# Kernel optimization log

Measured on AMD Instinct MI355X. Metric: run time of the kernel, lower is better.

## Reference

```python
import jax, jax.numpy as jnp
import numpy as np

HEADS = 16
DIM_HEAD = 64
SCALE = DIM_HEAD ** -0.5


def setup_inputs() -> dict:
    key = jax.random.key(0)
    k1, k2, k3, k4 = jax.random.split(key, 4)
    b, n, dim = 2, 2048, 1024
    inner = HEADS * DIM_HEAD  # 1024
    x = jax.random.normal(k1, (b, n, dim), dtype=jnp.float32)
    mask = jax.random.randint(k2, (b, n), 0, 2, dtype=jnp.int32)
    Wqkv = jax.random.normal(k3, (dim, inner), dtype=jnp.float32) * (dim ** -0.5)
    Wout = jax.random.normal(k4, (inner, dim), dtype=jnp.float32) * (inner ** -0.5)
    bout = jnp.zeros((dim,), dtype=jnp.float32)
    return {"x": x, "mask": mask, "Wqkv": Wqkv, "Wout": Wout, "bout": bout}


def reference(x, mask, Wqkv, Wout, bout):
    b, n, _ = x.shape
    # shared projection: w acts as q = k = v (CRATE subspace attention)
    w = jnp.einsum('bnd,de->bne', x, Wqkv)
    w = w.reshape(b, n, HEADS, DIM_HEAD).transpose(0, 2, 1, 3)  # b h n d
    dots = jnp.einsum('bhid,bhjd->bhij', w, w) * SCALE           # b h n n
    attn = jax.nn.softmax(dots, axis=-1)
    # post-softmax multiplicative masking (mask=1 zeros the column)
    m = mask[:, None, None, :].astype(attn.dtype)
    attn = attn * (1.0 - m)
    out = jnp.einsum('bhij,bhjd->bhid', attn, w)                 # b h n d
    out = out.transpose(0, 2, 1, 3).reshape(b, n, HEADS * DIM_HEAD)
    return jnp.einsum('bne,ed->bnd', out, Wout) + bout
```

## Files before the change

kernel.cpp:

```cpp
#include <hip/hip_runtime.h>
#include <hip/hip_bf16.h>
#include <stdint.h>

typedef unsigned short u16;
typedef unsigned int u32;
typedef __bf16 bf16x8 __attribute__((ext_vector_type(8)));
typedef float f32x4 __attribute__((ext_vector_type(4)));
typedef float f32x16 __attribute__((ext_vector_type(16)));
typedef u32 u32x4 __attribute__((ext_vector_type(4)));

#define AS1 __attribute__((address_space(1)))
#define AS3 __attribute__((address_space(3)))

__device__ __forceinline__ void async16(const u16* g, u16* l) {
  __builtin_amdgcn_global_load_lds((const AS1 uint32_t*)(const void*)g,
                                   (AS3 uint32_t*)l, 16, 0, 0);
}

__device__ __forceinline__ u16 f2bf(float v) {
  union { __hip_bfloat16 b; u16 u; } c; c.b = __float2bfloat16(v); return c.u;
}

__device__ __forceinline__ u32 pkbf(float a, float b) {
  u32 r;
  asm("v_cvt_pk_bf16_f32 %0, %1, %2" : "=v"(r) : "v"(a), "v"(b));
  return r;
}

__device__ __forceinline__ void swap32(u32 &a, u32 &b) {
  asm("v_permlane32_swap_b32 %0, %1" : "+v"(a), "+v"(b));
}

#if __has_builtin(__builtin_amdgcn_exp2f)
#define fast_exp2(x) __builtin_amdgcn_exp2f(x)
#else
#define fast_exp2(x) exp2f(x)
#endif

#if __has_builtin(__builtin_amdgcn_rcpf)
#define fast_rcp(x) __builtin_amdgcn_rcpf(x)
#else
#define fast_rcp(x) (1.0f / (x))
#endif

__device__ __forceinline__ uint4 pack8(float4 lo, float4 hi) {
  uint4 q;
  q.x = (u32)f2bf(lo.x) | ((u32)f2bf(lo.y) << 16);
  q.y = (u32)f2bf(lo.z) | ((u32)f2bf(lo.w) << 16);
  q.z = (u32)f2bf(hi.x) | ((u32)f2bf(hi.y) << 16);
  q.w = (u32)f2bf(hi.z) | ((u32)f2bf(hi.w) << 16);
  return q;
}

__global__ void prep(const float* __restrict__ x, u16* __restrict__ xb,
                     const float* __restrict__ Wqkv, u16* __restrict__ WqkvT,
                     const float* __restrict__ Wout, u16* __restrict__ WoutT) {
  const int tx = threadIdx.x, ty = threadIdx.y, z = blockIdx.z;
  if (z >= 2) {
    const int cid = (z - 2) * 256 + blockIdx.y * 16 + blockIdx.x;
    const int t = ty * 16 + tx;
    const int i = (cid * 256 + t) * 8;
    float4 lo = *(const float4*)(x + i);
    float4 hi = *(const float4*)(x + i + 4);
    *(uint4*)(xb + i) = pack8(lo, hi);
    return;
  }
  const float* in = z ? Wout : Wqkv;
  u16* out = z ? WoutT : WqkvT;
  __shared__ u16 tile[64][65];
  const int c0 = blockIdx.x * 64, r0 = blockIdx.y * 64;
#pragma unroll
  for (int i = 0; i < 4; i++) {
    const int row = r0 + ty + i * 16;
    float4 v = *(const float4*)&in[(size_t)row * 1024 + c0 + tx * 4];
    tile[tx * 4 + 0][ty + i * 16] = f2bf(v.x);
    tile[tx * 4 + 1][ty + i * 16] = f2bf(v.y);
    tile[tx * 4 + 2][ty + i * 16] = f2bf(v.z);
    tile[tx * 4 + 3][ty + i * 16] = f2bf(v.w);
  }
  __syncthreads();
#pragma unroll
  for (int i = 0; i < 4; i++) {
    const int orow = c0 + ty + i * 16;
    u32 w0 = (u32)tile[ty + i * 16][tx * 4 + 0] | ((u32)tile[ty + i * 16][tx * 4 + 1] << 16);
    u32 w1 = (u32)tile[ty + i * 16][tx * 4 + 2] | ((u32)tile[ty + i * 16][tx * 4 + 3] << 16);
    uint2 pk = {w0, w1};
    *(uint2*)&out[(size_t)orow * 1024 + r0 + tx * 4] = pk;
  }
}

__global__ void scale_transpose_v(const u16* __restrict__ w, const int* __restrict__ mask,
                                  u16* __restrict__ Vt) {
  __shared__ u16 tile[64][65];
  const int tx = threadIdx.x, ty = threadIdx.y;
  const int j0 = blockIdx.x * 64;
  const int bh = blockIdx.z, b = bh >> 4, hc = (bh & 15) * 64;
#pragma unroll
  for (int i = 0; i < 4; i++) {
    const int j = j0 + ty + i * 16;
    uint2 v = *(const uint2*)&w[(size_t)(b * 2048 + j) * 1024 + hc + tx * 4];
    if (mask[b * 2048 + j]) { v.x = 0u; v.y = 0u; }
    tile[tx * 4 + 0][ty + i * 16] = (u16)(v.x & 0xFFFF);
    tile[tx * 4 + 1][ty + i * 16] = (u16)(v.x >> 16);
    tile[tx * 4 + 2][ty + i * 16] = (u16)(v.y & 0xFFFF);
    tile[tx * 4 + 3][ty + i * 16] = (u16)(v.y >> 16);
  }
  __syncthreads();
#pragma unroll
  for (int i = 0; i < 4; i++) {
    const int d = ty + i * 16;
    u32 w0 = (u32)tile[d][tx * 4 + 0] | ((u32)tile[d][tx * 4 + 1] << 16);
    u32 w1 = (u32)tile[d][tx * 4 + 2] | ((u32)tile[d][tx * 4 + 3] << 16);
    uint2 pk = {w0, w1};
    *(uint2*)&Vt[((size_t)bh * 64 + d) * 2048 + j0 + tx * 4] = pk;
  }
}

template<bool OUT_F32>
__launch_bounds__(256)
__global__ void gemm_bt(const u16* __restrict__ A, const u16* __restrict__ BT,
                        void* __restrict__ Cp, const float* __restrict__ bias,
                        int M, int N, int K) {
  __shared__ __align__(16) u16 As[2][64 * 64];
  __shared__ __align__(16) u16 Bs[2][64 * 64];
  const int t = threadIdx.x;
  const int lane = t & 63, wave = t >> 6;
  const int ql = lane & 31, hi = lane >> 5, swz = ql & 7;
  const int wgid = blockIdx.x + gridDim.x * blockIdx.y;
  const int c = wgid & 7, ii = wgid >> 3;
  const int m0 = (c * 8 + (ii & 7)) * 64;
  const int n0 = (ii >> 3) * 64;
  const int wm = (wave & 1) * 32, wn = (wave >> 1) * 32;

  f32x16 acc = {};

  const int sr = t >> 3;
  const int sc8 = ((t & 7) ^ (sr & 7)) * 8;
  const u16* gAt = A + (size_t)(m0 + sr) * K + sc8;
  const u16* gBt = BT + (size_t)(n0 + sr) * K + sc8;

#define GSTAGE(buf, k0s) do { \
    async16(gAt + (k0s),                   &As[buf][t * 8]); \
    async16(gAt + (k0s) + (size_t)32 * K,  &As[buf][t * 8 + 2048]); \
    async16(gBt + (k0s),                   &Bs[buf][t * 8]); \
    async16(gBt + (k0s) + (size_t)32 * K,  &Bs[buf][t * 8 + 2048]); \
  } while (0)

  GSTAGE(0, 0);

  int cur = 0;
  for (int k0 = 0; k0 < K; k0 += 64) {
    if (k0 + 64 < K) {
      GSTAGE(cur ^ 1, k0 + 64);
      asm volatile("s_waitcnt vmcnt(4)" ::: "memory");
    } else {
      asm volatile("s_waitcnt vmcnt(0)" ::: "memory");
    }
    __builtin_amdgcn_s_barrier();
    __builtin_amdgcn_sched_barrier(0);

#pragma unroll
    for (int kk = 0; kk < 4; kk++) {
      bf16x8 af = *(const bf16x8*)&As[cur][(wm + ql) * 64 + (((2 * kk + hi) ^ swz) * 8)];
      bf16x8 bfr = *(const bf16x8*)&Bs[cur][(wn + ql) * 64 + (((2 * kk + hi) ^ swz) * 8)];
      acc = __builtin_amdgcn_mfma_f32_32x32x16_bf16(af, bfr, acc, 0, 0, 0);
    }
    asm volatile("s_waitcnt lgkmcnt(0)" ::: "memory");
    __builtin_amdgcn_sched_barrier(0);
    __builtin_amdgcn_s_barrier();
    __builtin_amdgcn_sched_barrier(0);
    cur ^= 1;
  }
#undef GSTAGE

  const float bv = bias ? bias[n0 + wn + ql] : 0.f;
  const int col = n0 + wn + ql;

#pragma unroll
  for (int r = 0; r < 16; r++) {
    const int row = m0 + wm + (r & 3) + 8 * (r >> 2) + 4 * hi;
    const size_t ci = (size_t)row * N + col;
    const float v = acc[r] + bv;
    if (OUT_F32) ((float*)Cp)[ci] = v;
    else ((u16*)Cp)[ci] = f2bf(v);
  }
}

#define C1 0.18033688f
#define C2 -28.853901f
__launch_bounds__(512)
__global__ void attn_kernel(const u16* __restrict__ w, const u16* __restrict__ Vt,
                            u16* __restrict__ y) {
  __shared__ __align__(16) u16 smem[2][2][2][64 * 64];
  const int t = threadIdx.x, lane = t & 63, wv = t >> 6;
  const int qg = wv & 3, kgr = wv >> 2;
  const int ql = lane & 31, hi = lane >> 5, swz = ql & 7;
  const int wgid = blockIdx.x + 16 * blockIdx.y;
  const int newid = (wgid & 7) * 64 + (wgid >> 3);
  const int bh = newid >> 4, b = bh >> 4, hc = (bh & 15) * 64;
  const int q0 = (newid & 15) * 128;
  const size_t rowb = (size_t)b * 2048;

  const int tt = t & 255;
  const int sg = t >> 8;
  const int skey = tt >> 3;
  const int scl = ((tt & 7) ^ (skey & 7)) * 8;
  const int sjb = sg * 1024;
  const u16* kptr = w + rowb * 1024 + hc;
  const u16* vptr = Vt + (size_t)bh * 64 * 2048;

  bf16x8 qf[4];
  {
    const size_t qrow = rowb + q0 + qg * 32 + ql;
#pragma unroll
    for (int ks = 0; ks < 4; ks++)
      qf[ks] = *(const bf16x8*)&w[qrow * 1024 + hc + ks * 16 + hi * 8];
  }

  union { u32x4 u; bf16x8 bf; } ones;
  ones.u = (u32x4){0x3F803F80u, 0x3F803F80u, 0x3F803F80u, 0x3F803F80u};

  f32x16 o0 = {}, o1 = {};
  f32x16 den = {};

#define STAGE(buf, j0s) do { \
    async16(kptr + (size_t)(sjb + (j0s) + skey) * 1024 + scl,       &smem[0][sg][buf][tt * 8]); \
    async16(kptr + (size_t)(sjb + (j0s) + skey + 32) * 1024 + scl,  &smem[0][sg][buf][2048 + tt * 8]); \
    async16(vptr + (size_t)skey * 2048 + sjb + (j0s) + scl,         &smem[1][sg][buf][tt * 8]); \
    async16(vptr + (size_t)(skey + 32) * 2048 + sjb + (j0s) + scl,  &smem[1][sg][buf][2048 + tt * 8]); \
  } while (0)

  STAGE(0, 0);
  __syncthreads();

  int cur = 0;
  for (int j0 = 0; j0 < 1024; j0 += 64) {
    if (j0 + 64 < 1024) STAGE(cur ^ 1, j0 + 64);

    const u16* Wt = smem[0][kgr][cur];
    const u16* Vts = smem[1][kgr][cur];

    u32x4 pa[4];
#pragma unroll
    for (int g = 0; g < 2; g++) {
      f32x16 p = {};
#pragma unroll
      for (int ks = 0; ks < 4; ks++) {
        bf16x8 af = *(const bf16x8*)
            &Wt[(g * 32 + ql) * 64 + (((ks * 2 + hi) ^ swz) * 8)];
        p = __builtin_amdgcn_mfma_f32_32x32x16_bf16(af, qf[ks], p, 0, 0, 0);
      }
      float e[16];
#pragma unroll
      for (int r = 0; r < 16; r++)
        e[r] = fast_exp2(fmaf(p[r], C1, C2));
      u32 a0 = pkbf(e[0], e[1]),   b0 = pkbf(e[4], e[5]);   swap32(a0, b0);
      u32 a1 = pkbf(e[2], e[3]),   b1 = pkbf(e[6], e[7]);   swap32(a1, b1);
      u32 a2 = pkbf(e[8], e[9]),   b2 = pkbf(e[12], e[13]); swap32(a2, b2);
      u32 a3 = pkbf(e[10], e[11]), b3 = pkbf(e[14], e[15]); swap32(a3, b3);
      u32x4 f0 = {a0, a1, b0, b1};
      u32x4 f1 = {a2, a3, b2, b3};
      pa[2 * g + 0] = f0;
      pa[2 * g + 1] = f1;
    }

    __builtin_amdgcn_s_setprio(1);
#pragma unroll
    for (int ks = 0; ks < 4; ks++) {
      union { u32x4 u; bf16x8 bf; } cv; cv.u = pa[ks];
      bf16x8 vb0 = *(const bf16x8*)
          &Vts[ql * 64 + (((ks * 2 + hi) ^ swz) * 8)];
      bf16x8 vb1 = *(const bf16x8*)
          &Vts[(32 + ql) * 64 + (((ks * 2 + hi) ^ swz) * 8)];
      o0 = __builtin_amdgcn_mfma_f32_32x32x16_bf16(cv.bf, vb0, o0, 0, 0, 0);
      o1 = __builtin_amdgcn_mfma_f32_32x32x16_bf16(cv.bf, vb1, o1, 0, 0, 0);
      den = __builtin_amdgcn_mfma_f32_32x32x16_bf16(cv.bf, ones.bf, den, 0, 0, 0);
    }
    __builtin_amdgcn_s_setprio(0);

    __syncthreads();
    cur ^= 1;
  }
#undef STAGE

  float* mrg = (float*)smem;
  float* slot = mrg + (qg * 64 + lane) * 49;
  if (kgr == 1) {
#pragma unroll
    for (int r = 0; r < 16; r++) {
      slot[r] = o0[r]; slot[16 + r] = o1[r]; slot[32 + r] = den[r];
    }
  }
  __syncthreads();
  if (kgr == 0) {
#pragma unroll
    for (int r = 0; r < 16; r++) {
      o0[r] += slot[r]; o1[r] += slot[16 + r]; den[r] += slot[32 + r];
    }
#pragma unroll
    for (int r = 0; r < 16; r++) {
      const int qo = (r & 3) + 8 * (r >> 2) + 4 * hi;
      const float iv = fast_rcp(den[r]);
      const size_t orow = rowb + q0 + qg * 32 + qo;
      y[orow * 1024 + hc + ql]      = f2bf(o0[r] * iv);
      y[orow * 1024 + hc + 32 + ql] = f2bf(o1[r] * iv);
    }
  }
}

extern "C" void kernel_launch(void* const* d_in, const int* in_sizes, int n_in,
                              void* d_out, int out_size, void* d_ws, size_t ws_size,
                              hipStream_t stream) {
  const float* x    = (const float*)d_in[0];
  const int* mask   = (const int*)d_in[1];
  const float* Wqkv = (const float*)d_in[2];
  const float* Wout = (const float*)d_in[3];
  const float* bout = (const float*)d_in[4];
  float* out = (float*)d_out;

  u16* w     = (u16*)d_ws;
  u16* y     = w + 4096 * 1024;
  u16* WqkvT = y + 4096 * 1024;
  u16* WoutT = WqkvT + 1024 * 1024;
  u16* Vt    = WoutT + 1024 * 1024;
  u16* xb    = y;

  prep<<<dim3(16, 16, 10), dim3(16, 16), 0, stream>>>(x, xb, Wqkv, WqkvT, Wout, WoutT);
  gemm_bt<false><<<dim3(64, 16), 256, 0, stream>>>(xb, WqkvT, w, nullptr, 4096, 1024, 1024);
  scale_transpose_v<<<dim3(32, 1, 32), dim3(16, 16), 0, stream>>>(w, mask, Vt);
  attn_kernel<<<dim3(16, 32), 512, 0, stream>>>(w, Vt, y);
  gemm_bt<true><<<dim3(64, 16), 256, 0, stream>>>(y, WoutT, out, bout, 4096, 1024, 1024);
}
```

Measured before the change: 158.2 us.

## Halve attention key tile to 32 and shrink LDS footprint

```diff
diff --git a/kernel.cpp b/kernel.cpp
--- a/kernel.cpp
+++ b/kernel.cpp
@@ -191,10 +191,11 @@
 __launch_bounds__(512)
 __global__ void attn_kernel(const u16* __restrict__ w, const u16* __restrict__ Vt,
                             u16* __restrict__ y) {
-  __shared__ __align__(16) u16 smem[2][2][2][64 * 64];
+  __shared__ __align__(16) u16 Ks[2][2][32 * 64];
+  __shared__ __align__(16) u16 Vs[2][2][64 * 32];
   const int t = threadIdx.x, lane = t & 63, wv = t >> 6;
   const int qg = wv & 3, kgr = wv >> 2;
-  const int ql = lane & 31, hi = lane >> 5, swz = ql & 7;
+  const int ql = lane & 31, hi = lane >> 5, swz = ql & 7, vswz = ql & 3;
   const int wgid = blockIdx.x + 16 * blockIdx.y;
   const int newid = (wgid & 7) * 64 + (wgid >> 3);
   const int bh = newid >> 4, b = bh >> 4, hc = (bh & 15) * 64;
@@ -205,6 +206,8 @@
   const int sg = t >> 8;
   const int skey = tt >> 3;
   const int scl = ((tt & 7) ^ (skey & 7)) * 8;
+  const int vd = tt >> 2;
+  const int vcl = ((tt & 3) ^ (vd & 3)) * 8;
   const int sjb = sg * 1024;
   const u16* kptr = w + rowb * 1024 + hc;
   const u16* vptr = Vt + (size_t)bh * 64 * 2048;
@@ -224,57 +227,50 @@
   f32x16 den = {};
 
 #define STAGE(buf, j0s) do { \
-    async16(kptr + (size_t)(sjb + (j0s) + skey) * 1024 + scl,       &smem[0][sg][buf][tt * 8]); \
-    async16(kptr + (size_t)(sjb + (j0s) + skey + 32) * 1024 + scl,  &smem[0][sg][buf][2048 + tt * 8]); \
-    async16(vptr + (size_t)skey * 2048 + sjb + (j0s) + scl,         &smem[1][sg][buf][tt * 8]); \
-    async16(vptr + (size_t)(skey + 32) * 2048 + sjb + (j0s) + scl,  &smem[1][sg][buf][2048 + tt * 8]); \
+    async16(kptr + (size_t)(sjb + (j0s) + skey) * 1024 + scl, &Ks[sg][buf][tt * 8]); \
+    async16(vptr + (size_t)vd * 2048 + sjb + (j0s) + vcl,     &Vs[sg][buf][tt * 8]); \
   } while (0)
 
   STAGE(0, 0);
   __syncthreads();
 
   int cur = 0;
-  for (int j0 = 0; j0 < 1024; j0 += 64) {
-    if (j0 + 64 < 1024) STAGE(cur ^ 1, j0 + 64);
-
-    const u16* Wt = smem[0][kgr][cur];
-    const u16* Vts = smem[1][kgr][cur];
-
-    u32x4 pa[4];
-#pragma unroll
-    for (int g = 0; g < 2; g++) {
-      f32x16 p = {};
-#pragma unroll
-      for (int ks = 0; ks < 4; ks++) {
-        bf16x8 af = *(const bf16x8*)
-            &Wt[(g * 32 + ql) * 64 + (((ks * 2 + hi) ^ swz) * 8)];
-        p = __builtin_amdgcn_mfma_f32_32x32x16_bf16(af, qf[ks], p, 0, 0, 0);
-      }
-      float e[16];
-#pragma unroll
-      for (int r = 0; r < 16; r++)
-        e[r] = fast_exp2(fmaf(p[r], C1, C2));
-      u32 a0 = pkbf(e[0], e[1]),   b0 = pkbf(e[4], e[5]);   swap32(a0, b0);
-      u32 a1 = pkbf(e[2], e[3]),   b1 = pkbf(e[6], e[7]);   swap32(a1, b1);
-      u32 a2 = pkbf(e[8], e[9]),   b2 = pkbf(e[12], e[13]); swap32(a2, b2);
-      u32 a3 = pkbf(e[10], e[11]), b3 = pkbf(e[14], e[15]); swap32(a3, b3);
-      u32x4 f0 = {a0, a1, b0, b1};
-      u32x4 f1 = {a2, a3, b2, b3};
-      pa[2 * g + 0] = f0;
-      pa[2 * g + 1] = f1;
-    }
+  for (int j0 = 0; j0 < 1024; j0 += 32) {
+    if (j0 + 32 < 1024) STAGE(cur ^ 1, j0 + 32);
+
+    const u16* Wt = Ks[kgr][cur];
+    const u16* Vts = Vs[kgr][cur];
+
+    f32x16 p = {};
+#pragma unroll
+    for (int ks = 0; ks < 4; ks++) {
+      bf16x8 af = *(const bf16x8*)&Wt[ql * 64 + (((ks * 2 + hi) ^ swz) * 8)];
+      p = __builtin_amdgcn_mfma_f32_32x32x16_bf16(af, qf[ks], p, 0, 0, 0);
+    }
+    float e[16];
+#pragma unroll
+    for (int r = 0; r < 16; r++)
+      e[r] = fast_exp2(fmaf(p[r], C1, C2));
+    u32 a0 = pkbf(e[0], e[1]),   b0 = pkbf(e[4], e[5]);   swap32(a0, b0);
+    u32 a1 = pkbf(e[2], e[3]),   b1 = pkbf(e[6], e[7]);   swap32(a1, b1);
+    u32 a2 = pkbf(e[8], e[9]),   b2 = pkbf(e[12], e[13]); swap32(a2, b2);
+    u32 a3 = pkbf(e[10], e[11]), b3 = pkbf(e[14], e[15]); swap32(a3, b3);
+    u32x4 pa0 = {a0, a1, b0, b1};
+    u32x4 pa1 = {a2, a3, b2, b3};
 
     __builtin_amdgcn_s_setprio(1);
-#pragma unroll
-    for (int ks = 0; ks < 4; ks++) {
-      union { u32x4 u; bf16x8 bf; } cv; cv.u = pa[ks];
-      bf16x8 vb0 = *(const bf16x8*)
-          &Vts[ql * 64 + (((ks * 2 + hi) ^ swz) * 8)];
-      bf16x8 vb1 = *(const bf16x8*)
-          &Vts[(32 + ql) * 64 + (((ks * 2 + hi) ^ swz) * 8)];
-      o0 = __builtin_amdgcn_mfma_f32_32x32x16_bf16(cv.bf, vb0, o0, 0, 0, 0);
-      o1 = __builtin_amdgcn_mfma_f32_32x32x16_bf16(cv.bf, vb1, o1, 0, 0, 0);
-      den = __builtin_amdgcn_mfma_f32_32x32x16_bf16(cv.bf, ones.bf, den, 0, 0, 0);
+    {
+      union { u32x4 u; bf16x8 bf; } c0, c1; c0.u = pa0; c1.u = pa1;
+      bf16x8 v00 = *(const bf16x8*)&Vts[ql * 32 + ((hi ^ vswz) * 8)];
+      bf16x8 v01 = *(const bf16x8*)&Vts[(32 + ql) * 32 + ((hi ^ vswz) * 8)];
+      bf16x8 v10 = *(const bf16x8*)&Vts[ql * 32 + (((2 + hi) ^ vswz) * 8)];
+      bf16x8 v11 = *(const bf16x8*)&Vts[(32 + ql) * 32 + (((2 + hi) ^ vswz) * 8)];
+      o0 = __builtin_amdgcn_mfma_f32_32x32x16_bf16(c0.bf, v00, o0, 0, 0, 0);
+      o1 = __builtin_amdgcn_mfma_f32_32x32x16_bf16(c0.bf, v01, o1, 0, 0, 0);
+      den = __builtin_amdgcn_mfma_f32_32x32x16_bf16(c0.bf, ones.bf, den, 0, 0, 0);
+      o0 = __builtin_amdgcn_mfma_f32_32x32x16_bf16(c1.bf, v10, o0, 0, 0, 0);
+      o1 = __builtin_amdgcn_mfma_f32_32x32x16_bf16(c1.bf, v11, o1, 0, 0, 0);
+      den = __builtin_amdgcn_mfma_f32_32x32x16_bf16(c1.bf, ones.bf, den, 0, 0, 0);
     }
     __builtin_amdgcn_s_setprio(0);
 
@@ -283,27 +279,32 @@
   }
 #undef STAGE
 
-  float* mrg = (float*)smem;
-  float* slot = mrg + (qg * 64 + lane) * 49;
-  if (kgr == 1) {
-#pragma unroll
-    for (int r = 0; r < 16; r++) {
-      slot[r] = o0[r]; slot[16 + r] = o1[r]; slot[32 + r] = den[r];
-    }
-  }
-  __syncthreads();
+  float* mrg = (float*)Ks;
+  float* slot = mrg + (qg * 64 + lane) * 17;
+  f32x16 om0 = o0, om1 = o1, dm = den;
+#define MERGE(vec) do { \
+    if (kgr == 1) { \
+      _Pragma("unroll") for (int r = 0; r < 16; r++) slot[r] = (vec)[r]; \
+    } \
+    __syncthreads(); \
+    if (kgr == 0) { \
+      _Pragma("unroll") for (int r = 0; r < 16; r++) (vec)[r] += slot[r]; \
+    } \
+    __syncthreads(); \
+  } while (0)
+  MERGE(om0);
+  MERGE(om1);
+  MERGE(dm);
+#undef MERGE
+
   if (kgr == 0) {
-#pragma unroll
-    for (int r = 0; r < 16; r++) {
-      o0[r] += slot[r]; o1[r] += slot[16 + r]; den[r] += slot[32 + r];
-    }
 #pragma unroll
     for (int r = 0; r < 16; r++) {
       const int qo = (r & 3) + 8 * (r >> 2) + 4 * hi;
-      const float iv = fast_rcp(den[r]);
+      const float iv = fast_rcp(dm[r]);
       const size_t orow = rowb + q0 + qg * 32 + qo;
-      y[orow * 1024 + hc + ql]      = f2bf(o0[r] * iv);
-      y[orow * 1024 + hc + 32 + ql] = f2bf(o1[r] * iv);
+      y[orow * 1024 + hc + ql]      = f2bf(om0[r] * iv);
+      y[orow * 1024 + hc + 32 + ql] = f2bf(om1[r] * iv);
     }
   }
 }
```

Result: no change. 160.5 us (+1.4%).

## Enlarge GEMM tiles to 128x128 with 2x2 MFMA accumulators per wave

Applied to the files above, without the earlier changes.

```diff
diff --git a/kernel.cpp b/kernel.cpp
--- a/kernel.cpp
+++ b/kernel.cpp
@@ -121,18 +121,18 @@
 __global__ void gemm_bt(const u16* __restrict__ A, const u16* __restrict__ BT,
                         void* __restrict__ Cp, const float* __restrict__ bias,
                         int M, int N, int K) {
-  __shared__ __align__(16) u16 As[2][64 * 64];
-  __shared__ __align__(16) u16 Bs[2][64 * 64];
+  __shared__ __align__(16) u16 As[2][128 * 64];
+  __shared__ __align__(16) u16 Bs[2][128 * 64];
   const int t = threadIdx.x;
   const int lane = t & 63, wave = t >> 6;
   const int ql = lane & 31, hi = lane >> 5, swz = ql & 7;
   const int wgid = blockIdx.x + gridDim.x * blockIdx.y;
   const int c = wgid & 7, ii = wgid >> 3;
-  const int m0 = (c * 8 + (ii & 7)) * 64;
-  const int n0 = (ii >> 3) * 64;
-  const int wm = (wave & 1) * 32, wn = (wave >> 1) * 32;
-
-  f32x16 acc = {};
+  const int m0 = (c * 4 + (ii & 3)) * 128;
+  const int n0 = (ii >> 2) * 128;
+  const int wr = (wave & 1) * 64, wc = (wave >> 1) * 64;
+
+  f32x16 acc[2][2] = {};
 
   const int sr = t >> 3;
   const int sc8 = ((t & 7) ^ (sr & 7)) * 8;
@@ -142,8 +142,12 @@
 #define GSTAGE(buf, k0s) do { \
     async16(gAt + (k0s),                   &As[buf][t * 8]); \
     async16(gAt + (k0s) + (size_t)32 * K,  &As[buf][t * 8 + 2048]); \
+    async16(gAt + (k0s) + (size_t)64 * K,  &As[buf][t * 8 + 4096]); \
+    async16(gAt + (k0s) + (size_t)96 * K,  &As[buf][t * 8 + 6144]); \
     async16(gBt + (k0s),                   &Bs[buf][t * 8]); \
     async16(gBt + (k0s) + (size_t)32 * K,  &Bs[buf][t * 8 + 2048]); \
+    async16(gBt + (k0s) + (size_t)64 * K,  &Bs[buf][t * 8 + 4096]); \
+    async16(gBt + (k0s) + (size_t)96 * K,  &Bs[buf][t * 8 + 6144]); \
   } while (0)
 
   GSTAGE(0, 0);
@@ -152,7 +156,7 @@
   for (int k0 = 0; k0 < K; k0 += 64) {
     if (k0 + 64 < K) {
       GSTAGE(cur ^ 1, k0 + 64);
-      asm volatile("s_waitcnt vmcnt(4)" ::: "memory");
+      asm volatile("s_waitcnt vmcnt(8)" ::: "memory");
     } else {
       asm volatile("s_waitcnt vmcnt(0)" ::: "memory");
     }
@@ -161,9 +165,15 @@
 
 #pragma unroll
     for (int kk = 0; kk < 4; kk++) {
-      bf16x8 af = *(const bf16x8*)&As[cur][(wm + ql) * 64 + (((2 * kk + hi) ^ swz) * 8)];
-      bf16x8 bfr = *(const bf16x8*)&Bs[cur][(wn + ql) * 64 + (((2 * kk + hi) ^ swz) * 8)];
-      acc = __builtin_amdgcn_mfma_f32_32x32x16_bf16(af, bfr, acc, 0, 0, 0);
+      const int ch = ((2 * kk + hi) ^ swz) * 8;
+      bf16x8 af0 = *(const bf16x8*)&As[cur][(wr + ql) * 64 + ch];
+      bf16x8 af1 = *(const bf16x8*)&As[cur][(wr + 32 + ql) * 64 + ch];
+      bf16x8 bf0 = *(const bf16x8*)&Bs[cur][(wc + ql) * 64 + ch];
+      bf16x8 bf1 = *(const bf16x8*)&Bs[cur][(wc + 32 + ql) * 64 + ch];
+      acc[0][0] = __builtin_amdgcn_mfma_f32_32x32x16_bf16(af0, bf0, acc[0][0], 0, 0, 0);
+      acc[0][1] = __builtin_amdgcn_mfma_f32_32x32x16_bf16(af0, bf1, acc[0][1], 0, 0, 0);
+      acc[1][0] = __builtin_amdgcn_mfma_f32_32x32x16_bf16(af1, bf0, acc[1][0], 0, 0, 0);
+      acc[1][1] = __builtin_amdgcn_mfma_f32_32x32x16_bf16(af1, bf1, acc[1][1], 0, 0, 0);
     }
     asm volatile("s_waitcnt lgkmcnt(0)" ::: "memory");
     __builtin_amdgcn_sched_barrier(0);
@@ -173,16 +183,26 @@
   }
 #undef GSTAGE
 
-  const float bv = bias ? bias[n0 + wn + ql] : 0.f;
-  const int col = n0 + wn + ql;
-
-#pragma unroll
-  for (int r = 0; r < 16; r++) {
-    const int row = m0 + wm + (r & 3) + 8 * (r >> 2) + 4 * hi;
-    const size_t ci = (size_t)row * N + col;
-    const float v = acc[r] + bv;
-    if (OUT_F32) ((float*)Cp)[ci] = v;
-    else ((u16*)Cp)[ci] = f2bf(v);
+  float bv[2] = {0.f, 0.f};
+  if (bias) {
+    bv[0] = bias[n0 + wc + ql];
+    bv[1] = bias[n0 + wc + 32 + ql];
+  }
+
+#pragma unroll
+  for (int I = 0; I < 2; I++) {
+#pragma unroll
+    for (int r = 0; r < 16; r++) {
+      const int row = m0 + wr + I * 32 + (r & 3) + 8 * (r >> 2) + 4 * hi;
+#pragma unroll
+      for (int J = 0; J < 2; J++) {
+        const int col = n0 + wc + J * 32 + ql;
+        const size_t ci = (size_t)row * N + col;
+        const float v = acc[I][J][r] + bv[J];
+        if (OUT_F32) ((float*)Cp)[ci] = v;
+        else ((u16*)Cp)[ci] = f2bf(v);
+      }
+    }
   }
 }
 
@@ -326,8 +346,8 @@
   u16* xb    = y;
 
   prep<<<dim3(16, 16, 10), dim3(16, 16), 0, stream>>>(x, xb, Wqkv, WqkvT, Wout, WoutT);
-  gemm_bt<false><<<dim3(64, 16), 256, 0, stream>>>(xb, WqkvT, w, nullptr, 4096, 1024, 1024);
+  gemm_bt<false><<<dim3(32, 8), 256, 0, stream>>>(xb, WqkvT, w, nullptr, 4096, 1024, 1024);
   scale_transpose_v<<<dim3(32, 1, 32), dim3(16, 16), 0, stream>>>(w, mask, Vt);
   attn_kernel<<<dim3(16, 32), 512, 0, stream>>>(w, Vt, y);
-  gemm_bt<true><<<dim3(64, 16), 256, 0, stream>>>(y, WoutT, out, bout, 4096, 1024, 1024);
-}
+  gemm_bt<true><<<dim3(32, 8), 256, 0, stream>>>(y, WoutT, out, bout, 4096, 1024, 1024);
+}
```

Result: slower. 164.5 us (+3.9%).
